# Optimization experiments

Hardware: AMD Instinct MI355X
Metric: run time of the kernel (lower is better)

## Reference

```python
import jax, jax.numpy as jnp
import numpy as np

NEG_SLOPE = 0.2  # PyG GATConv default negative_slope


def gat_conv(x, src, dst, W, att_src, att_dst, bias, heads):
    """PyG-style GATConv (concat=True). src/dst already include self-loops.
    x: [N, Fin]; W: [Fin, heads*Fout]; att_*: [heads, Fout]; bias: [heads*Fout].
    """
    N = x.shape[0]
    Fout = att_src.shape[-1]
    h = (x @ W).reshape(N, heads, Fout)              # [N, H, C]
    a_s = jnp.einsum('nhc,hc->nh', h, att_src)        # [N, H]
    a_d = jnp.einsum('nhc,hc->nh', h, att_dst)        # [N, H]
    e = jax.nn.leaky_relu(a_s[src] + a_d[dst], NEG_SLOPE)   # [E, H]
    # segment softmax over destination nodes
    m = jax.lax.stop_gradient(jax.ops.segment_max(e, dst, num_segments=N))  # [N, H]
    ex = jnp.exp(e - m[dst])
    denom = jax.ops.segment_sum(ex, dst, num_segments=N)     # [N, H]
    alpha = ex / (denom[dst] + 1e-16)                          # [E, H]
    msg = h[src] * alpha[:, :, None]                           # [E, H, C]
    out = jax.ops.segment_sum(msg, dst, num_segments=N)       # [N, H, C]
    return out.reshape(N, heads * Fout) + bias


def setup_inputs() -> dict:
    key = jax.random.key(0)
    ks = jax.random.split(key, 16)
    NU, NS, D, H, CTX, B, E = 100000, 100000, 64, 2, 3, 512, 1600000
    inp = {
        'user_idx': jax.random.randint(ks[0], (B,), 0, NU),
        'context_idx': jax.random.randint(ks[1], (B, CTX), 0, NS),
        'edge_index': jax.random.randint(ks[2], (2, E), 0, NS),
        'user_emb': jax.random.normal(ks[3], (NU, D), jnp.float32),
        'service_emb': jax.random.normal(ks[4], (NS, D), jnp.float32),
        'W1': jax.random.normal(ks[5], (D, H * D), jnp.float32) / np.sqrt(D),
        'att_src1': jax.random.normal(ks[6], (H, D), jnp.float32) / np.sqrt(D),
        'att_dst1': jax.random.normal(ks[7], (H, D), jnp.float32) / np.sqrt(D),
        'b1': jnp.zeros((H * D,), jnp.float32),
        'W2': jax.random.normal(ks[8], (H * D, D), jnp.float32) / np.sqrt(H * D),
        'att_src2': jax.random.normal(ks[9], (1, D), jnp.float32) / np.sqrt(D),
        'att_dst2': jax.random.normal(ks[10], (1, D), jnp.float32) / np.sqrt(D),
        'b2': jnp.zeros((D,), jnp.float32),
        'fc_w': jax.random.normal(ks[11], (D * (CTX + 1), NS), jnp.float32) / np.sqrt(D * (CTX + 1)),
        'fc_b': jnp.zeros((NS,), jnp.float32),
    }
    return inp


def reference(user_idx, context_idx, edge_index, user_emb, service_emb,
              W1, att_src1, att_dst1, b1, W2, att_src2, att_dst2, b2, fc_w, fc_b):
    N = service_emb.shape[0]
    loops = jnp.arange(N)
    src = jnp.concatenate([edge_index[0], loops])  # add self loops (PyG default)
    dst = jnp.concatenate([edge_index[1], loops])
    user_vec = user_emb[user_idx]                                  # [B, D]
    g = gat_conv(service_emb, src, dst, W1, att_src1, att_dst1, b1, heads=2)
    g = jax.nn.elu(g)
    g = gat_conv(g, src, dst, W2, att_src2, att_dst2, b2, heads=1)  # [N, D]
    ctx = g[context_idx]                                            # [B, CTX, D]
    ctx = ctx.reshape(ctx.shape[0], -1)
    x = jnp.concatenate([user_vec, ctx], axis=1)                    # [B, D*(CTX+1)]
    return x @ fc_w + fc_b                                           # [B, num_services]
```

## Files before the change

kernel.cpp:

```cpp
#include <hip/hip_runtime.h>
#include <hip/hip_bf16.h>
#include <math.h>

#define NEG_SLOPE 0.2f

#define NPB 512
#define NPB_SH 9
#define SRC_BITS 18
#define LCAP 16384
#define BCAP 16384

typedef __attribute__((ext_vector_type(8))) short short8;
typedef __attribute__((ext_vector_type(4))) float f32x4;

__device__ __forceinline__ float leaky(float x) { return x > 0.f ? x : NEG_SLOPE * x; }

__device__ __forceinline__ unsigned short f2bf(float f) {
  unsigned u = __float_as_uint(f);
  unsigned r = (u + 0x7FFFu + ((u >> 16) & 1u)) >> 16;
  return (unsigned short)r;
}

__global__ void k_h1(const float* __restrict__ x, const float* __restrict__ W1,
                     const float* __restrict__ att_src, const float* __restrict__ att_dst,
                     unsigned short* __restrict__ h1, float* __restrict__ a_s,
                     float* __restrict__ a_d, int N) {
  __shared__ __align__(16) float W1s[64 * 128];
  __shared__ __align__(16) float xs[32][64];
  const int tid = threadIdx.x;
  for (int i = tid; i < 64 * 128; i += 256) W1s[i] = W1[i];
  const int node0 = blockIdx.x * 32;
  for (int i = tid; i < 512; i += 256) {
    const int nn = node0 + (i >> 4);
    if (nn < N) ((float4*)xs)[i] = *(const float4*)(x + (size_t)nn * 64 + (i & 15) * 4);
  }
  const int ln  = tid >> 7;
  const int col = tid & 127;
  const int head = col >> 6;
  const int c = col & 63;
  const float as_w = att_src[head * 64 + c];
  const float ad_w = att_dst[head * 64 + c];
  __syncthreads();
  float wreg[64];
#pragma unroll
  for (int cc = 0; cc < 64; ++cc) wreg[cc] = W1s[cc * 128 + col];

  for (int it = 0; it < 16; ++it) {
    const int slot = it * 2 + ln;
    const int n = node0 + slot;
    if (n >= N) continue;
    float acc = 0.f;
#pragma unroll
    for (int q = 0; q < 16; ++q) {
      const float4 xv = *(const float4*)&xs[slot][q * 4];
      acc = fmaf(xv.x, wreg[q * 4 + 0], acc);
      acc = fmaf(xv.y, wreg[q * 4 + 1], acc);
      acc = fmaf(xv.z, wreg[q * 4 + 2], acc);
      acc = fmaf(xv.w, wreg[q * 4 + 3], acc);
    }
    h1[(size_t)n * 128 + col] = f2bf(acc);
    float vs = acc * as_w;
    float vd = acc * ad_w;
#pragma unroll
    for (int off = 32; off > 0; off >>= 1) {
      vs += __shfl_down(vs, off, 64);
      vd += __shfl_down(vd, off, 64);
    }
    if (c == 0) { a_s[n * 2 + head] = vs; a_d[n * 2 + head] = vd; }
  }
}

__global__ void k_init(int* __restrict__ cursor, int NB, int* __restrict__ flagC,
                       int* __restrict__ flag1, int* __restrict__ cnt, int N) {
  const int i = blockIdx.x * 256 + threadIdx.x;
  if (i < NB) cursor[i] = i * BCAP;
  if (i < N) { flagC[i] = 0; flag1[i] = 0; }
  if (i < 2) cnt[i] = 0;
}

__global__ __launch_bounds__(1024) void k_bscatter(const int* __restrict__ src,
                                                   const int* __restrict__ dst, int E, int Etot,
                                                   int epb, int* __restrict__ cursor,
                                                   unsigned* __restrict__ rec, int NB) {
  __shared__ int hist[256];
  __shared__ int cur[256];
  const int tid = threadIdx.x;
  if (tid < 256) hist[tid] = 0;
  __syncthreads();
  const int e0 = blockIdx.x * epb;
  const int e1 = min(e0 + epb, Etot);
  for (int e = e0 + tid; e < e1; e += 1024) {
    const int d = (e < E) ? dst[e] : (e - E);
    atomicAdd(&hist[d >> NPB_SH], 1);
  }
  __syncthreads();
  if (tid < NB) {
    const int c = hist[tid];
    cur[tid] = c ? atomicAdd(&cursor[tid], c) : 0;
  }
  __syncthreads();
  for (int e = e0 + tid; e < e1; e += 1024) {
    int sv, d;
    if (e < E) { sv = src[e]; d = dst[e]; } else { sv = d = e - E; }
    const int b = d >> NPB_SH;
    const int p = atomicAdd(&cur[b], 1);
    rec[p] = (unsigned)sv | ((unsigned)(d & (NPB - 1)) << SRC_BITS);
  }
}

__global__ void k_bscan2(const int* __restrict__ cursor, int* __restrict__ bucketBase,
                         int NB, int Etot, int* __restrict__ rowptr, int N) {
  __shared__ int s[256];
  const int tid = threadIdx.x;
  const int v = (tid < NB) ? (cursor[tid] - tid * BCAP) : 0;
  s[tid] = v;
  __syncthreads();
  for (int off = 1; off < 256; off <<= 1) {
    const int t = (tid >= off) ? s[tid - off] : 0;
    __syncthreads();
    s[tid] += t;
    __syncthreads();
  }
  if (tid < NB) bucketBase[tid] = s[tid] - v;
  if (tid == 0) { bucketBase[NB] = Etot; rowptr[N] = Etot; }
}

__global__ __launch_bounds__(1024) void k_bcsr(const unsigned* __restrict__ rec,
                                               const int* __restrict__ bucketBase,
                                               int* __restrict__ rowptr, int* __restrict__ adj,
                                               int N, int NB) {
  __shared__ int ldeg[NPB];
  __shared__ int s[NPB];
  __shared__ int ladj[LCAP];
  const int b = blockIdx.x;
  const int tid = threadIdx.x;
  const int o0 = bucketBase[b];
  const int cnt = bucketBase[b + 1] - o0;
  const int r0 = b * BCAP;
  if (tid < NPB) ldeg[tid] = 0;
  __syncthreads();
  for (int i = tid; i < cnt; i += 1024)
    atomicAdd(&ldeg[rec[r0 + i] >> SRC_BITS], 1);
  __syncthreads();
  int v = 0;
  if (tid < NPB) { v = ldeg[tid]; s[tid] = v; }
  __syncthreads();
  for (int off = 1; off < NPB; off <<= 1) {
    int t = 0;
    if (tid < NPB && tid >= off) t = s[tid - off];
    __syncthreads();
    if (tid < NPB) s[tid] += t;
    __syncthreads();
  }
  if (tid < NPB) {
    const int excl = s[tid] - v;
    const int node = b * NPB + tid;
    if (node < N) rowptr[node] = o0 + excl;
    ldeg[tid] = excl;
  }
  __syncthreads();
  if (cnt <= LCAP) {
    for (int i = tid; i < cnt; i += 1024) {
      const unsigned r = rec[r0 + i];
      const int p = atomicAdd(&ldeg[r >> SRC_BITS], 1);
      ladj[p] = (int)(r & ((1u << SRC_BITS) - 1));
    }
    __syncthreads();
    for (int i = tid; i < cnt; i += 1024) adj[o0 + i] = ladj[i];
  } else {
    for (int i = tid; i < cnt; i += 1024) {
      const unsigned r = rec[r0 + i];
      const int p = atomicAdd(&ldeg[r >> SRC_BITS], 1);
      adj[o0 + p] = (int)(r & ((1u << SRC_BITS) - 1));
    }
  }
}

__global__ void k_markC(const int* __restrict__ ctx, int nctx, int* __restrict__ flagC,
                        int* __restrict__ flag1, int* __restrict__ listC,
                        int* __restrict__ list1, int* __restrict__ cnt) {
  const int i = blockIdx.x * 256 + threadIdx.x;
  if (i >= nctx) return;
  const int n = ctx[i];
  if (atomicExch(&flagC[n], 1) == 0) {
    listC[atomicAdd(&cnt[0], 1)] = n;
    if (atomicExch(&flag1[n], 1) == 0)
      list1[atomicAdd(&cnt[1], 1)] = n;
  }
}

__global__ void k_markS1(const int* __restrict__ listC, const int* __restrict__ rowptr,
                         const int* __restrict__ adj, int* __restrict__ flag1,
                         int* __restrict__ list1, int* __restrict__ cnt) {
  const int i = blockIdx.x * 256 + threadIdx.x;
  if (i >= cnt[0]) return;
  const int n = listC[i];
  const int kb = rowptr[n], ke = rowptr[n + 1];
  for (int k = kb; k < ke; ++k) {
    const int s = adj[k];
    if (atomicExch(&flag1[s], 1) == 0)
      list1[atomicAdd(&cnt[1], 1)] = s;
  }
}

__global__ void k_gat1(const unsigned short* __restrict__ h1, const float* __restrict__ as1,
                       const float* __restrict__ ad1, const int* __restrict__ rowptr,
                       const int* __restrict__ adj, const float* __restrict__ b1,
                       float* __restrict__ g, const int* __restrict__ list1,
                       const int* __restrict__ cnt) {
  const int w = threadIdx.x >> 6;
  const int l = threadIdx.x & 63;
  const int idx = blockIdx.x * 4 + w;
  if (idx >= cnt[1]) return;
  const int n = list1[idx];
  const int half = l >> 5;
  const int q = l & 31;
  const int head = q >> 4;
  const float adh = ad1[n * 2 + head];
  float a0 = 0.f, a1 = 0.f, a2 = 0.f, a3 = 0.f, dsum = 0.f;
  const int kb = rowptr[n], ke = rowptr[n + 1];
  const int kend = ke - 1;
  for (int k = kb + half; k < ke; k += 8) {
    const int e1 = k + 2, e2 = k + 4, e3 = k + 6;
    const int s0 = adj[k];
    const int s1 = adj[min(e1, kend)];
    const int s2 = adj[min(e2, kend)];
    const int s3 = adj[min(e3, kend)];
    const float x0 = as1[s0 * 2 + head] + adh;
    const float x1 = as1[s1 * 2 + head] + adh;
    const float x2 = as1[s2 * 2 + head] + adh;
    const float x3 = as1[s3 * 2 + head] + adh;
    const uint2 u0 = *(const uint2*)(h1 + (size_t)s0 * 128 + 4 * q);
    const uint2 u1 = *(const uint2*)(h1 + (size_t)s1 * 128 + 4 * q);
    const uint2 u2 = *(const uint2*)(h1 + (size_t)s2 * 128 + 4 * q);
    const uint2 u3 = *(const uint2*)(h1 + (size_t)s3 * 128 + 4 * q);
    const float w0 = __expf(leaky(x0));
    const float w1 = (e1 < ke) ? __expf(leaky(x1)) : 0.f;
    const float w2 = (e2 < ke) ? __expf(leaky(x2)) : 0.f;
    const float w3 = (e3 < ke) ? __expf(leaky(x3)) : 0.f;
    dsum += (w0 + w1) + (w2 + w3);
    a0 = fmaf(w0, __uint_as_float(u0.x << 16), a0);
    a1 = fmaf(w0, __uint_as_float(u0.x & 0xFFFF0000u), a1);
    a2 = fmaf(w0, __uint_as_float(u0.y << 16), a2);
    a3 = fmaf(w0, __uint_as_float(u0.y & 0xFFFF0000u), a3);
    a0 = fmaf(w1, __uint_as_float(u1.x << 16), a0);
    a1 = fmaf(w1, __uint_as_float(u1.x & 0xFFFF0000u), a1);
    a2 = fmaf(w1, __uint_as_float(u1.y << 16), a2);
    a3 = fmaf(w1, __uint_as_float(u1.y & 0xFFFF0000u), a3);
    a0 = fmaf(w2, __uint_as_float(u2.x << 16), a0);
    a1 = fmaf(w2, __uint_as_float(u2.x & 0xFFFF0000u), a1);
    a2 = fmaf(w2, __uint_as_float(u2.y << 16), a2);
    a3 = fmaf(w2, __uint_as_float(u2.y & 0xFFFF0000u), a3);
    a0 = fmaf(w3, __uint_as_float(u3.x << 16), a0);
    a1 = fmaf(w3, __uint_as_float(u3.x & 0xFFFF0000u), a1);
    a2 = fmaf(w3, __uint_as_float(u3.y << 16), a2);
    a3 = fmaf(w3, __uint_as_float(u3.y & 0xFFFF0000u), a3);
  }
  a0 += __shfl_xor(a0, 32, 64);
  a1 += __shfl_xor(a1, 32, 64);
  a2 += __shfl_xor(a2, 32, 64);
  a3 += __shfl_xor(a3, 32, 64);
  dsum += __shfl_xor(dsum, 32, 64);
  if (half == 0) {
    const float inv = 1.f / (dsum + 1e-16f);
    const float4 bv = *(const float4*)(b1 + 4 * q);
    float g0 = fmaf(a0, inv, bv.x);
    float g1 = fmaf(a1, inv, bv.y);
    float g2v = fmaf(a2, inv, bv.z);
    float g3 = fmaf(a3, inv, bv.w);
    g0 = g0 > 0.f ? g0 : expm1f(g0);
    g1 = g1 > 0.f ? g1 : expm1f(g1);
    g2v = g2v > 0.f ? g2v : expm1f(g2v);
    g3 = g3 > 0.f ? g3 : expm1f(g3);
    *(float4*)(g + (size_t)n * 128 + 4 * q) = make_float4(g0, g1, g2v, g3);
  }
}

__global__ void k_h2(const float* __restrict__ g, const float* __restrict__ W2,
                     const float* __restrict__ att_s, const float* __restrict__ att_d,
                     unsigned short* __restrict__ h2, float* __restrict__ a_s,
                     float* __restrict__ a_d, const int* __restrict__ list1,
                     const int* __restrict__ cnt) {
  const int cnt1 = cnt[1];
  const int base0 = blockIdx.x * 32;
  if (base0 >= cnt1) return;
  __shared__ __align__(16) float W2s[128 * 64];
  __shared__ __align__(16) float gs[2][128];
  __shared__ float part[2][64];
  for (int i = threadIdx.x; i < 128 * 64; i += 256) W2s[i] = W2[i];
  const int col = threadIdx.x & 63;
  const int kh  = (threadIdx.x >> 6) & 1;
  const int ln  = threadIdx.x >> 7;
  const float as_w = att_s[col], ad_w = att_d[col];
  __syncthreads();
  float wreg[64];
#pragma unroll
  for (int cc = 0; cc < 64; ++cc) wreg[cc] = W2s[(kh * 64 + cc) * 64 + col];

  for (int it = 0; it < 16; ++it) {
    const int sbase = base0 + it * 2;
    __syncthreads();
    {
      const int slot = sbase + (threadIdx.x >> 7);
      if (slot < cnt1) {
        const int nn = list1[slot];
        gs[threadIdx.x >> 7][threadIdx.x & 127] = g[(size_t)nn * 128 + (threadIdx.x & 127)];
      }
    }
    __syncthreads();
    const int slot = sbase + ln;
    const int n = (slot < cnt1) ? list1[slot] : -1;
    float acc = 0.f;
    if (n >= 0) {
#pragma unroll
      for (int q = 0; q < 16; ++q) {
        const float4 gv = *(const float4*)&gs[ln][kh * 64 + q * 4];
        acc = fmaf(gv.x, wreg[q * 4 + 0], acc);
        acc = fmaf(gv.y, wreg[q * 4 + 1], acc);
        acc = fmaf(gv.z, wreg[q * 4 + 2], acc);
        acc = fmaf(gv.w, wreg[q * 4 + 3], acc);
      }
    }
    if (kh == 1) part[ln][col] = acc;
    __syncthreads();
    if (kh == 0 && n >= 0) {
      acc += part[ln][col];
      h2[(size_t)n * 64 + col] = f2bf(acc);
      float vs = acc * as_w, vd = acc * ad_w;
#pragma unroll
      for (int off = 32; off > 0; off >>= 1) {
        vs += __shfl_down(vs, off, 64);
        vd += __shfl_down(vd, off, 64);
      }
      if (col == 0) { a_s[n] = vs; a_d[n] = vd; }
    }
  }
}

__global__ void k_gat2(const unsigned short* __restrict__ h2, const float* __restrict__ as2,
                       const float* __restrict__ ad2, const int* __restrict__ rowptr,
                       const int* __restrict__ adj, const float* __restrict__ b2,
                       float* __restrict__ g2, const int* __restrict__ listC,
                       const int* __restrict__ cnt) {
  const int w = threadIdx.x >> 6;
  const int l = threadIdx.x & 63;
  const int idx = blockIdx.x * 4 + w;
  if (idx >= cnt[0]) return;
  const int n = listC[idx];
  const int half = l >> 5;
  const int q = l & 31;
  const float adh = ad2[n];
  float a0 = 0.f, a1 = 0.f, dsum = 0.f;
  const int kb = rowptr[n], ke = rowptr[n + 1];
  const int kend = ke - 1;
  for (int k = kb + half; k < ke; k += 8) {
    const int e1 = k + 2, e2 = k + 4, e3 = k + 6;
    const int s0 = adj[k];
    const int s1 = adj[min(e1, kend)];
    const int s2 = adj[min(e2, kend)];
    const int s3 = adj[min(e3, kend)];
    const float x0 = as2[s0] + adh;
    const float x1 = as2[s1] + adh;
    const float x2 = as2[s2] + adh;
    const float x3 = as2[s3] + adh;
    const unsigned u0 = *(const unsigned*)(h2 + (size_t)s0 * 64 + 2 * q);
    const unsigned u1 = *(const unsigned*)(h2 + (size_t)s1 * 64 + 2 * q);
    const unsigned u2 = *(const unsigned*)(h2 + (size_t)s2 * 64 + 2 * q);
    const unsigned u3 = *(const unsigned*)(h2 + (size_t)s3 * 64 + 2 * q);
    const float w0 = __expf(leaky(x0));
    const float w1 = (e1 < ke) ? __expf(leaky(x1)) : 0.f;
    const float w2 = (e2 < ke) ? __expf(leaky(x2)) : 0.f;
    const float w3 = (e3 < ke) ? __expf(leaky(x3)) : 0.f;
    dsum += (w0 + w1) + (w2 + w3);
    a0 = fmaf(w0, __uint_as_float(u0 << 16), a0);
    a1 = fmaf(w0, __uint_as_float(u0 & 0xFFFF0000u), a1);
    a0 = fmaf(w1, __uint_as_float(u1 << 16), a0);
    a1 = fmaf(w1, __uint_as_float(u1 & 0xFFFF0000u), a1);
    a0 = fmaf(w2, __uint_as_float(u2 << 16), a0);
    a1 = fmaf(w2, __uint_as_float(u2 & 0xFFFF0000u), a1);
    a0 = fmaf(w3, __uint_as_float(u3 << 16), a0);
    a1 = fmaf(w3, __uint_as_float(u3 & 0xFFFF0000u), a1);
  }
  a0 += __shfl_xor(a0, 32, 64);
  a1 += __shfl_xor(a1, 32, 64);
  dsum += __shfl_xor(dsum, 32, 64);
  if (half == 0) {
    const float inv = 1.f / (dsum + 1e-16f);
    const float2 bv = *(const float2*)(b2 + 2 * q);
    ((float2*)g2)[(size_t)n * 32 + q] =
        make_float2(fmaf(a0, inv, bv.x), fmaf(a1, inv, bv.y));
  }
}

__global__ void k_xmat(const int* __restrict__ user_idx, const int* __restrict__ ctx_idx,
                       const float* __restrict__ user_emb, const float* __restrict__ g2,
                       unsigned short* __restrict__ xb) {
  const int b = blockIdx.x;
  const int k = threadIdx.x;
  float v;
  if (k < 64) {
    v = user_emb[(size_t)user_idx[b] * 64 + k];
  } else {
    const int c = (k - 64) >> 6;
    v = g2[(size_t)ctx_idx[b * 3 + c] * 64 + (k & 63)];
  }
  xb[(size_t)(k >> 5) * (512 * 32) + b * 32 + (k & 31)] = f2bf(v);
}

__global__ __launch_bounds__(512) void k_fc(const unsigned short* __restrict__ xb,
                                            const float* __restrict__ fc_w,
                                            const float* __restrict__ fc_b,
                                            float* __restrict__ out, int NSRV,
                                            int ntiles, int gstride) {
  __shared__ __align__(16) unsigned short Blds[2][32 * 264];

  const int tid = threadIdx.x;
  const int w = tid >> 6;
  const int lane = tid & 63;
  const int l15 = lane & 15;
  const int kg = lane >> 4;

  if (blockIdx.x >= (unsigned)ntiles) return;

  short8 afr[4][8];
#pragma unroll
  for (int mf = 0; mf < 4; ++mf) {
    const int row = w * 64 + mf * 16 + l15;
#pragma unroll
    for (int ks = 0; ks < 8; ++ks) {
      afr[mf][ks] = *(const short8*)(xb + (size_t)ks * 16384 + row * 32 + kg * 8);
    }
  }

  const int sc = tid & 31;
  const int sk = tid >> 5;

  float v[16];
  auto loadv = [&](int t) {
    const int cg = t * 32 + sc;
    const bool okc = cg < NSRV;
#pragma unroll
    for (int i = 0; i < 16; ++i)
      v[i] = okc ? __builtin_nontemporal_load(fc_w + (size_t)(sk + i * 16) * NSRV + cg) : 0.f;
  };
  auto writev = [&](int buf) {
#pragma unroll
    for (int i = 0; i < 16; ++i)
      Blds[buf][sc * 264 + sk + i * 16] = f2bf(v[i]);
  };

  loadv(blockIdx.x);
  writev(0);
  if (blockIdx.x + gstride < ntiles) loadv(blockIdx.x + gstride);
  __syncthreads();

  int cur = 0;
  for (int t = blockIdx.x; t < ntiles; t += gstride) {
    if (t + gstride < ntiles) writev(cur ^ 1);
    if (t + 2 * gstride < ntiles) loadv(t + 2 * gstride);
    const int j0 = t * 32;
#pragma unroll
    for (int nf = 0; nf < 2; ++nf) {
      short8 bfr[8];
#pragma unroll
      for (int ks = 0; ks < 8; ++ks)
        bfr[ks] = *(const short8*)&Blds[cur][(nf * 16 + l15) * 264 + ks * 32 + kg * 8];
      f32x4 acc[4];
#pragma unroll
      for (int mf = 0; mf < 4; ++mf) acc[mf] = (f32x4){0.f, 0.f, 0.f, 0.f};
#pragma unroll
      for (int ks = 0; ks < 8; ++ks)
#pragma unroll
        for (int mf = 0; mf < 4; ++mf)
          acc[mf] = __builtin_amdgcn_mfma_f32_16x16x32_bf16(bfr[ks], afr[mf][ks], acc[mf], 0, 0, 0);
      const int jc = j0 + nf * 16 + kg * 4;
      if (j0 + 32 <= NSRV) {
        const float4 bias = *(const float4*)(fc_b + jc);
#pragma unroll
        for (int mf = 0; mf < 4; ++mf) {
          const int row = w * 64 + mf * 16 + l15;
          f32x4 o;
          o[0] = acc[mf][0] + bias.x;
          o[1] = acc[mf][1] + bias.y;
          o[2] = acc[mf][2] + bias.z;
          o[3] = acc[mf][3] + bias.w;
          __builtin_nontemporal_store(o, (f32x4*)(out + (size_t)row * NSRV + jc));
        }
      } else {
#pragma unroll
        for (int mf = 0; mf < 4; ++mf) {
          const int row = w * 64 + mf * 16 + l15;
#pragma unroll
          for (int r = 0; r < 4; ++r) {
            const int j = jc + r;
            if (j < NSRV) out[(size_t)row * NSRV + j] = acc[mf][r] + fc_b[j];
          }
        }
      }
    }
    __syncthreads();
    cur ^= 1;
  }
}

extern "C" void kernel_launch(void* const* d_in, const int* in_sizes, int n_in,
                              void* d_out, int out_size, void* d_ws, size_t ws_size,
                              hipStream_t stream) {
  const int* user_idx    = (const int*)d_in[0];
  const int* context_idx = (const int*)d_in[1];
  const int* edge_index  = (const int*)d_in[2];
  const float* user_emb  = (const float*)d_in[3];
  const float* service_emb = (const float*)d_in[4];
  const float* W1        = (const float*)d_in[5];
  const float* att_src1  = (const float*)d_in[6];
  const float* att_dst1  = (const float*)d_in[7];
  const float* b1        = (const float*)d_in[8];
  const float* W2        = (const float*)d_in[9];
  const float* att_src2  = (const float*)d_in[10];
  const float* att_dst2  = (const float*)d_in[11];
  const float* b2        = (const float*)d_in[12];
  const float* fc_w      = (const float*)d_in[13];
  const float* fc_b      = (const float*)d_in[14];
  float* out = (float*)d_out;

  const int B    = in_sizes[0];
  const int E    = in_sizes[2] / 2;
  const int N    = in_sizes[4] / 64;
  const int NSRV = in_sizes[14];
  const int Etot = E + N;
  const int NCTX = in_sizes[1];
  (void)B;

  const int* edge_src = edge_index;
  const int* edge_dst = edge_index + E;

  char* ws = (char*)d_ws;
  size_t off = 0;
  auto alloc = [&](size_t bytes) {
    void* p = ws + off;
    off = (off + bytes + 255) & ~(size_t)255;
    return p;
  };
  const int NB = (N + NPB - 1) >> NPB_SH;
  unsigned short* h1 = (unsigned short*)alloc((size_t)N * 128 * 2);
  float* g      = (float*)alloc((size_t)N * 128 * 4);
  float* as1    = (float*)alloc((size_t)N * 2 * 4);
  float* ad1    = (float*)alloc((size_t)N * 2 * 4);
  float* as2    = (float*)alloc((size_t)N * 4);
  float* ad2    = (float*)alloc((size_t)N * 4);
  int*   rowptr = (int*)alloc((size_t)(N + 1) * 4);
  int*   adj    = (int*)alloc((size_t)Etot * 4);
  unsigned* rec = (unsigned*)alloc((size_t)NB * BCAP * 4);
  int* bucketBase   = (int*)alloc(257 * 4);
  int* bucketCursor = (int*)alloc(256 * 4);
  int* flagC  = (int*)alloc((size_t)N * 4);
  int* flag1  = (int*)alloc((size_t)N * 4);
  int* listC  = (int*)alloc((size_t)NCTX * 4);
  int* list1  = (int*)alloc((size_t)N * 4);
  int* cnt    = (int*)alloc(2 * 4);
  unsigned short* xb = (unsigned short*)alloc((size_t)512 * 256 * 2);
  unsigned short* h2 = h1;
  float* g2 = g;
  (void)ws_size;

  const int NBLK2 = 256;
  const int epb = (Etot + NBLK2 - 1) / NBLK2;
  const int nblk_N = (N + 255) / 256;

  k_init<<<nblk_N, 256, 0, stream>>>(bucketCursor, NB, flagC, flag1, cnt, N);

  k_h1<<<(N + 31) / 32, 256, 0, stream>>>(service_emb, W1, att_src1, att_dst1, h1, as1, ad1, N);

  k_bscatter<<<NBLK2, 1024, 0, stream>>>(edge_src, edge_dst, E, Etot, epb, bucketCursor, rec, NB);
  k_bscan2<<<1, 256, 0, stream>>>(bucketCursor, bucketBase, NB, Etot, rowptr, N);
  k_bcsr<<<NB, 1024, 0, stream>>>(rec, bucketBase, rowptr, adj, N, NB);

  k_markC<<<(NCTX + 255) / 256, 256, 0, stream>>>(context_idx, NCTX, flagC, flag1, listC, list1, cnt);
  k_markS1<<<(NCTX + 255) / 256, 256, 0, stream>>>(listC, rowptr, adj, flag1, list1, cnt);

  k_gat1<<<(N + 3) / 4, 256, 0, stream>>>(h1, as1, ad1, rowptr, adj, b1, g, list1, cnt);

  k_h2<<<(N + 31) / 32, 256, 0, stream>>>(g, W2, att_src2, att_dst2, h2, as2, ad2, list1, cnt);

  k_gat2<<<(NCTX + 3) / 4, 256, 0, stream>>>(h2, as2, ad2, rowptr, adj, b2, g2, listC, cnt);

  k_xmat<<<512, 256, 0, stream>>>(user_idx, context_idx, user_emb, g2, xb);

  const int nfct = (NSRV + 31) / 32;
  const int grid = 512;
  k_fc<<<grid, 512, 0, stream>>>(xb, fc_w, fc_b, out, NSRV, nfct, grid);
}
```

Baseline: 295.5 us.

## Mark needed nodes from raw edges and build CSR only for layer-1 nodes

Context and first-hop source nodes are now found with a scan over the raw edge list, which happens before the CSR build. The bucket scatter then keeps only edges whose destination is flagged as needed, so the CSR holds just the rows used by the two GAT layers. This cuts the scatter and CSR work and the memory traffic, at the cost of one extra full pass over the edges with flag lookups. The FC grid size is also doubled.

```diff
diff --git a/kernel.cpp b/kernel.cpp
--- a/kernel.cpp
+++ b/kernel.cpp
@@ -78,9 +78,37 @@
   if (i < 2) cnt[i] = 0;
 }
 
+__global__ void k_markC(const int* __restrict__ ctx, int nctx, int* __restrict__ flagC,
+                        int* __restrict__ flag1, int* __restrict__ listC,
+                        int* __restrict__ list1, int* __restrict__ cnt) {
+  const int i = blockIdx.x * 256 + threadIdx.x;
+  if (i >= nctx) return;
+  const int n = ctx[i];
+  if (atomicExch(&flagC[n], 1) == 0) {
+    listC[atomicAdd(&cnt[0], 1)] = n;
+    if (atomicExch(&flag1[n], 1) == 0)
+      list1[atomicAdd(&cnt[1], 1)] = n;
+  }
+}
+
+__global__ void k_markS1e(const int* __restrict__ src, const int* __restrict__ dst,
+                          int E, int Etot, const int* __restrict__ flagC,
+                          int* __restrict__ flag1, int* __restrict__ list1,
+                          int* __restrict__ cnt) {
+  const int e = blockIdx.x * 256 + threadIdx.x;
+  if (e >= Etot) return;
+  int s, d;
+  if (e < E) { s = src[e]; d = dst[e]; } else { s = d = e - E; }
+  if (flagC[d]) {
+    if (atomicExch(&flag1[s], 1) == 0)
+      list1[atomicAdd(&cnt[1], 1)] = s;
+  }
+}
+
 __global__ __launch_bounds__(1024) void k_bscatter(const int* __restrict__ src,
                                                    const int* __restrict__ dst, int E, int Etot,
-                                                   int epb, int* __restrict__ cursor,
+                                                   int epb, const int* __restrict__ flag1,
+                                                   int* __restrict__ cursor,
                                                    unsigned* __restrict__ rec, int NB) {
   __shared__ int hist[256];
   __shared__ int cur[256];
@@ -91,7 +119,7 @@
   const int e1 = min(e0 + epb, Etot);
   for (int e = e0 + tid; e < e1; e += 1024) {
     const int d = (e < E) ? dst[e] : (e - E);
-    atomicAdd(&hist[d >> NPB_SH], 1);
+    if (flag1[d]) atomicAdd(&hist[d >> NPB_SH], 1);
   }
   __syncthreads();
   if (tid < NB) {
@@ -102,6 +130,7 @@
   for (int e = e0 + tid; e < e1; e += 1024) {
     int sv, d;
     if (e < E) { sv = src[e]; d = dst[e]; } else { sv = d = e - E; }
+    if (!flag1[d]) continue;
     const int b = d >> NPB_SH;
     const int p = atomicAdd(&cur[b], 1);
     rec[p] = (unsigned)sv | ((unsigned)(d & (NPB - 1)) << SRC_BITS);
@@ -109,7 +138,7 @@
 }
 
 __global__ void k_bscan2(const int* __restrict__ cursor, int* __restrict__ bucketBase,
-                         int NB, int Etot, int* __restrict__ rowptr, int N) {
+                         int NB, int* __restrict__ rowptr, int N) {
   __shared__ int s[256];
   const int tid = threadIdx.x;
   const int v = (tid < NB) ? (cursor[tid] - tid * BCAP) : 0;
@@ -122,7 +151,7 @@
     __syncthreads();
   }
   if (tid < NB) bucketBase[tid] = s[tid] - v;
-  if (tid == 0) { bucketBase[NB] = Etot; rowptr[N] = Etot; }
+  if (tid == 0) { bucketBase[NB] = s[255]; rowptr[N] = s[255]; }
 }
 
 __global__ __launch_bounds__(1024) void k_bcsr(const unsigned* __restrict__ rec,
@@ -173,33 +202,6 @@
       const int p = atomicAdd(&ldeg[r >> SRC_BITS], 1);
       adj[o0 + p] = (int)(r & ((1u << SRC_BITS) - 1));
     }
-  }
-}
-
-__global__ void k_markC(const int* __restrict__ ctx, int nctx, int* __restrict__ flagC,
-                        int* __restrict__ flag1, int* __restrict__ listC,
-                        int* __restrict__ list1, int* __restrict__ cnt) {
-  const int i = blockIdx.x * 256 + threadIdx.x;
-  if (i >= nctx) return;
-  const int n = ctx[i];
-  if (atomicExch(&flagC[n], 1) == 0) {
-    listC[atomicAdd(&cnt[0], 1)] = n;
-    if (atomicExch(&flag1[n], 1) == 0)
-      list1[atomicAdd(&cnt[1], 1)] = n;
-  }
-}
-
-__global__ void k_markS1(const int* __restrict__ listC, const int* __restrict__ rowptr,
-                         const int* __restrict__ adj, int* __restrict__ flag1,
-                         int* __restrict__ list1, int* __restrict__ cnt) {
-  const int i = blockIdx.x * 256 + threadIdx.x;
-  if (i >= cnt[0]) return;
-  const int n = listC[i];
-  const int kb = rowptr[n], ke = rowptr[n + 1];
-  for (int k = kb; k < ke; ++k) {
-    const int s = adj[k];
-    if (atomicExch(&flag1[s], 1) == 0)
-      list1[atomicAdd(&cnt[1], 1)] = s;
   }
 }
 
@@ -566,18 +568,19 @@
   const int NBLK2 = 256;
   const int epb = (Etot + NBLK2 - 1) / NBLK2;
   const int nblk_N = (N + 255) / 256;
+  const int nblk_E = (Etot + 255) / 256;
 
   k_init<<<nblk_N, 256, 0, stream>>>(bucketCursor, NB, flagC, flag1, cnt, N);
 
   k_h1<<<(N + 31) / 32, 256, 0, stream>>>(service_emb, W1, att_src1, att_dst1, h1, as1, ad1, N);
 
-  k_bscatter<<<NBLK2, 1024, 0, stream>>>(edge_src, edge_dst, E, Etot, epb, bucketCursor, rec, NB);
-  k_bscan2<<<1, 256, 0, stream>>>(bucketCursor, bucketBase, NB, Etot, rowptr, N);
+  k_markC<<<(NCTX + 255) / 256, 256, 0, stream>>>(context_idx, NCTX, flagC, flag1, listC, list1, cnt);
+  k_markS1e<<<nblk_E, 256, 0, stream>>>(edge_src, edge_dst, E, Etot, flagC, flag1, list1, cnt);
+
+  k_bscatter<<<NBLK2, 1024, 0, stream>>>(edge_src, edge_dst, E, Etot, epb, flag1, bucketCursor, rec, NB);
+  k_bscan2<<<1, 256, 0, stream>>>(bucketCursor, bucketBase, NB, rowptr, N);
   k_bcsr<<<NB, 1024, 0, stream>>>(rec, bucketBase, rowptr, adj, N, NB);
 
-  k_markC<<<(NCTX + 255) / 256, 256, 0, stream>>>(context_idx, NCTX, flagC, flag1, listC, list1, cnt);
-  k_markS1<<<(NCTX + 255) / 256, 256, 0, stream>>>(listC, rowptr, adj, flag1, list1, cnt);
-
   k_gat1<<<(N + 3) / 4, 256, 0, stream>>>(h1, as1, ad1, rowptr, adj, b1, g, list1, cnt);
 
   k_h2<<<(N + 31) / 32, 256, 0, stream>>>(g, W2, att_src2, att_dst2, h2, as2, ad2, list1, cnt);
@@ -587,6 +590,6 @@
   k_xmat<<<512, 256, 0, stream>>>(user_idx, context_idx, user_emb, g2, xb);
 
   const int nfct = (NSRV + 31) / 32;
-  const int grid = 512;
+  const int grid = 1024;
   k_fc<<<grid, 512, 0, stream>>>(xb, fc_w, fc_b, out, NSRV, nfct, grid);
 }
```

Result: slower. 430.9 us (+45.8%).
